# Kernel tuning notes

Measured on AMD Instinct MI355X. Metric: run time of the kernel, lower is better.

## Reference

```python
import jax, jax.numpy as jnp
import numpy as np
from jax import lax

LATENT_DIM = 512
TOKEN_DIM = 256
KERNEL = 5
STRIDE = 5


def setup_inputs() -> dict:
    key = jax.random.key(0)
    ks = jax.random.split(key, 8)
    B, L, S = 8, 1024, 10240
    s = lambda fan_in: 1.0 / np.sqrt(fan_in)
    return {
        "latents": jax.random.normal(ks[0], (B, L, LATENT_DIM), dtype=jnp.float32),
        "tokens": jax.random.normal(ks[1], (B, S, TOKEN_DIM), dtype=jnp.float32),
        # nn.Linear weights, stored as (out, in) like torch
        "W_lat": jax.random.uniform(ks[2], (LATENT_DIM, LATENT_DIM), jnp.float32, -s(LATENT_DIM), s(LATENT_DIM)),
        "W_tok": jax.random.uniform(ks[3], (LATENT_DIM, LATENT_DIM), jnp.float32, -s(LATENT_DIM), s(LATENT_DIM)),
        "W_vlat": jax.random.uniform(ks[4], (LATENT_DIM, LATENT_DIM), jnp.float32, -s(LATENT_DIM), s(LATENT_DIM)),
        "W_vtok": jax.random.uniform(ks[5], (LATENT_DIM, LATENT_DIM), jnp.float32, -s(LATENT_DIM), s(LATENT_DIM)),
        # Conv1d weight (out_ch, in_ch, k) and bias
        "conv_w": jax.random.uniform(ks[6], (LATENT_DIM, TOKEN_DIM, KERNEL), jnp.float32, -s(TOKEN_DIM * KERNEL), s(TOKEN_DIM * KERNEL)),
        "conv_b": jax.random.uniform(ks[7], (LATENT_DIM,), jnp.float32, -s(TOKEN_DIM * KERNEL), s(TOKEN_DIM * KERNEL)),
    }


def reference(latents, tokens, W_lat, W_tok, W_vlat, W_vtok, conv_w, conv_b):
    # Conv1d: (B,S,token_dim) -> (B,S//5,latent_dim)
    tok = lax.conv_general_dilated(
        tokens.transpose(0, 2, 1), conv_w, window_strides=(STRIDE,),
        padding="VALID", dimension_numbers=("NCH", "OIH", "NCH"))
    tok = (tok + conv_b[None, :, None]).transpose(0, 2, 1)  # (B, S', D)

    R_lat = jnp.einsum("bld,ed->ble", latents, W_lat)
    R_tok = jnp.einsum("bsd,ed->bse", tok, W_tok)
    V_lat = jnp.einsum("bld,ed->ble", latents, W_vlat)
    V_tok = jnp.einsum("bsd,ed->bse", tok, W_vtok)

    # shared score matrix, used for both row-wise and column-wise softmax
    A = jnp.einsum("ble,bse->bls", R_lat, R_tok) / jnp.sqrt(jnp.float32(LATENT_DIM))
    delta_lat = jnp.einsum("bls,bse->ble", jax.nn.softmax(A, axis=-1), V_tok)
    delta_tok = jnp.einsum("bls,ble->bse", jax.nn.softmax(A, axis=1), V_lat)

    updated_latents = latents + delta_lat
    updated_tokens = tok + delta_tok
    output = jnp.concatenate([updated_latents, updated_tokens], axis=1)
    return (updated_latents, updated_tokens, output)
```

## Files before the change

### kernel.cpp

```cpp
#include <hip/hip_runtime.h>
#include <math.h>

#define SCALEF 0.044194173824159216f

typedef __attribute__((ext_vector_type(8))) short bf16x8;
typedef __attribute__((ext_vector_type(4))) float f32x4;

static __device__ __forceinline__ unsigned short f2bf(float f) {
    union { float f; unsigned int i; } v; v.f = f;
    return (unsigned short)((v.i + 0x7fffu + ((v.i >> 16) & 1u)) >> 16);
}
static __device__ __forceinline__ float bf2f(unsigned short h) {
    union { unsigned int i; float f; } v; v.i = ((unsigned int)h) << 16;
    return v.f;
}
static __device__ __forceinline__ void gload16(const void* g, void* l) {
    __builtin_amdgcn_global_load_lds(
        (const __attribute__((address_space(1))) unsigned int*)g,
        (__attribute__((address_space(3))) unsigned int*)l, 16, 0, 0);
}
static __device__ __forceinline__ int swz(int l, int n) {
    return (l & 7) * (n >> 3) + (l >> 3);
}

__global__ __launch_bounds__(256) void cvt_tl(const float4* __restrict__ tok,
                                              const float4* __restrict__ lat,
                                              ushort4* __restrict__ tokd,
                                              ushort4* __restrict__ latd) {
    long t = blockIdx.x * 256L + threadIdx.x;
    #pragma unroll
    for (int k = 0; k < 5; ++k) {
        long i = t + k * 1048576L;
        float4 f = tok[i];
        ushort4 u; u.x = f2bf(f.x); u.y = f2bf(f.y); u.z = f2bf(f.z); u.w = f2bf(f.w);
        tokd[i] = u;
    }
    {
        float4 f = lat[t];
        ushort4 u; u.x = f2bf(f.x); u.y = f2bf(f.y); u.z = f2bf(f.z); u.w = f2bf(f.w);
        latd[t] = u;
    }
}

__global__ __launch_bounds__(256) void prep_rest(
    const float4* __restrict__ wl, const float4* __restrict__ wt,
    const float4* __restrict__ wvl, const float4* __restrict__ wvt,
    const float* __restrict__ cw,
    ushort4* __restrict__ wlb, ushort4* __restrict__ wtb,
    ushort4* __restrict__ wvlb, ushort4* __restrict__ wvtb,
    unsigned int* __restrict__ wpb)
{
    const long NW = 65536, NCV = 327680;
    for (long i = blockIdx.x * 256L + threadIdx.x; i < 4 * NW + NCV;
         i += gridDim.x * 256L) {
        long r = i;
        const float4* s = nullptr; ushort4* d = nullptr;
        if (r < NW) { s = wl; d = wlb; }
        else if ((r -= NW) < NW) { s = wt; d = wtb; }
        else if ((r -= NW) < NW) { s = wvl; d = wvlb; }
        else if ((r -= NW) < NW) { s = wvt; d = wvtb; }
        else {
            r -= NW;
            long e = r / 640, rr = r % 640, k = rr >> 7, c2 = rr & 127;
            unsigned int lo = f2bf(cw[e * 1280 + (2 * c2) * 5 + k]);
            unsigned int hi = f2bf(cw[e * 1280 + (2 * c2 + 1) * 5 + k]);
            wpb[r] = lo | (hi << 16);
            continue;
        }
        float4 f = s[r];
        ushort4 u; u.x = f2bf(f.x); u.y = f2bf(f.y); u.z = f2bf(f.z); u.w = f2bf(f.w);
        d[r] = u;
    }
}

template<int RL>
static __device__ __forceinline__ void sm_body(unsigned short* __restrict__ rowp,
                                               float* __restrict__ redm,
                                               float* __restrict__ reds) {
    constexpr int U = RL / 512;
    unsigned int* p = (unsigned int*)rowp;
    const int t = threadIdx.x, lane = t & 63, wid = t >> 6;
    unsigned int u[U];
    float v[2 * U];
    #pragma unroll
    for (int i = 0; i < U; ++i) u[i] = p[t + (i << 8)];
    #pragma unroll
    for (int i = 0; i < U; ++i) {
        v[2 * i]     = bf2f((unsigned short)(u[i] & 0xffffu));
        v[2 * i + 1] = bf2f((unsigned short)(u[i] >> 16));
    }
    float m = -INFINITY;
    #pragma unroll
    for (int i = 0; i < 2 * U; ++i) m = fmaxf(m, v[i]);
    #pragma unroll
    for (int k = 1; k < 64; k <<= 1) m = fmaxf(m, __shfl_xor(m, k));
    if (lane == 0) redm[wid] = m;
    __syncthreads();
    m = fmaxf(fmaxf(redm[0], redm[1]), fmaxf(redm[2], redm[3]));
    float s = 0.f, e[2 * U];
    #pragma unroll
    for (int i = 0; i < 2 * U; ++i) { e[i] = __expf(v[i] - m); s += e[i]; }
    #pragma unroll
    for (int k = 1; k < 64; k <<= 1) s += __shfl_xor(s, k);
    if (lane == 0) reds[wid] = s;
    __syncthreads();
    s = reds[0] + reds[1] + reds[2] + reds[3];
    float inv = 1.f / s;
    #pragma unroll
    for (int i = 0; i < U; ++i) {
        unsigned int lo = f2bf(e[2 * i] * inv);
        unsigned int hi = f2bf(e[2 * i + 1] * inv);
        p[t + (i << 8)] = lo | (hi << 16);
    }
}

__global__ __launch_bounds__(256) void softmax_both(unsigned short* __restrict__ S,
                                                    unsigned short* __restrict__ ST) {
    __shared__ float redm[4], reds[4];
    long b = blockIdx.x;
    if (b < 8192) sm_body<2048>(S + b * 2048L, redm, reds);
    else          sm_body<1024>(ST + (b - 8192) * 1024L, redm, reds);
}

template<int AMODE, int EPI>
static __device__ __forceinline__ void mm_body(
    char* __restrict__ smc, int bx, int by, int z,
    const unsigned short* __restrict__ A, const unsigned short* __restrict__ B,
    long bsA, long bsB, int lda, int ldb, int K,
    unsigned short* __restrict__ Cb, long bsCb,
    float* __restrict__ C0, long bsC0, float* __restrict__ C1, long bsC1,
    const void* __restrict__ basep, long bsBase, int ldc, float scale)
{
    const int t = threadIdx.x, lane = t & 63, wid = t >> 6;
    const int m0 = by << 7, n0 = bx << 7;
    const unsigned short* Ab = A + (long)z * bsA;
    const unsigned short* Bb = B + (long)z * bsB;

    const int rA0 = wid * 16 + (lane >> 2);
    const int rA1 = rA0 + 64;
    const int cs0 = (lane & 3) ^ ((rA0 >> 1) & 3);
    const int cs1 = (lane & 3) ^ ((rA1 >> 1) & 3);

    long aoff0, aoff1;
    if (AMODE == 0) {
        aoff0 = (long)(m0 + rA0) * lda + cs0 * 8;
        aoff1 = (long)(m0 + rA1) * lda + cs1 * 8;
    } else {
        int ma = m0 + rA0, mb = m0 + rA1;
        aoff0 = (long)(ma >> 11) * 2621440 + (long)(ma & 2047) * 1280 + cs0 * 8;
        aoff1 = (long)(mb >> 11) * 2621440 + (long)(mb & 2047) * 1280 + cs1 * 8;
    }
    const long boff0 = (long)(n0 + rA0) * ldb + cs0 * 8;
    const long boff1 = (long)(n0 + rA1) * ldb + cs1 * 8;

    const int dA0 = (wid << 10), dA1 = ((wid + 4) << 10);
    const int dB0 = 8192 + (wid << 10), dB1 = 8192 + ((wid + 4) << 10);

    const int wr = wid >> 1, wc = wid & 1;
    const int l15 = lane & 15, cslot = lane >> 4;
    int offA[4], offB[4];
    #pragma unroll
    for (int i = 0; i < 4; ++i) {
        int r = wr * 64 + i * 16 + l15;
        offA[i] = r * 64 + ((cslot ^ ((r >> 1) & 3)) << 4);
        int rb = wc * 64 + i * 16 + l15;
        offB[i] = 8192 + rb * 64 + ((cslot ^ ((rb >> 1) & 3)) << 4);
    }

    f32x4 acc[4][4];
    #pragma unroll
    for (int i = 0; i < 4; ++i)
        #pragma unroll
        for (int j = 0; j < 4; ++j)
            acc[i][j] = (f32x4)(0.f);

#define STAGE(p, ktv) do {                                   \
        int kb_ = (ktv);                                     \
        int bo_ = (p) * 16384;                               \
        gload16(Ab + aoff0 + kb_, smc + bo_ + dA0);          \
        gload16(Ab + aoff1 + kb_, smc + bo_ + dA1);          \
        gload16(Bb + boff0 + kb_, smc + bo_ + dB0);          \
        gload16(Bb + boff1 + kb_, smc + bo_ + dB1);          \
    } while (0)

    const int nt = K >> 5;
    STAGE(0, 0);
    STAGE(1, 32);
    int cur = 0;
    for (int it = 0; it < nt; ++it) {
        if (it + 2 < nt) {
            int nx2 = (cur >= 1) ? cur - 1 : 2;
            STAGE(nx2, (it + 2) << 5);
            asm volatile("s_waitcnt vmcnt(8)" ::: "memory");
        } else if (it + 1 < nt) {
            asm volatile("s_waitcnt vmcnt(4)" ::: "memory");
        } else {
            asm volatile("s_waitcnt vmcnt(0)" ::: "memory");
        }
        __builtin_amdgcn_s_barrier();
        const char* base = smc + cur * 16384;
        bf16x8 af[4], bfr[4];
        #pragma unroll
        for (int i = 0; i < 4; ++i) af[i]  = *(const bf16x8*)(base + offA[i]);
        #pragma unroll
        for (int i = 0; i < 4; ++i) bfr[i] = *(const bf16x8*)(base + offB[i]);
        #pragma unroll
        for (int i = 0; i < 4; ++i)
            #pragma unroll
            for (int j = 0; j < 4; ++j)
                acc[i][j] = __builtin_amdgcn_mfma_f32_16x16x32_bf16(af[i], bfr[j], acc[i][j], 0, 0, 0);
        asm volatile("s_waitcnt lgkmcnt(0)" ::: "memory");
        __builtin_amdgcn_s_barrier();
        cur = (cur + 1 == 3) ? 0 : cur + 1;
    }
#undef STAGE

    const int colb = n0 + wc * 64 + l15;
    const int rowb = m0 + wr * 64 + cslot * 4;
    if (EPI == 4) {
        unsigned short* STp = (unsigned short*)C0;
        #pragma unroll
        for (int i = 0; i < 4; ++i) {
            #pragma unroll
            for (int j = 0; j < 4; ++j) {
                int n = colb + j * 16;
                int mb = rowb + i * 16;
                float v0 = acc[i][j][0] * scale, v1 = acc[i][j][1] * scale;
                float v2 = acc[i][j][2] * scale, v3 = acc[i][j][3] * scale;
                unsigned short b0 = f2bf(v0), b1 = f2bf(v1), b2 = f2bf(v2), b3 = f2bf(v3);
                unsigned short* sp = Cb + (long)z * bsCb + (long)mb * ldc + n;
                sp[0] = b0; sp[ldc] = b1; sp[2 * ldc] = b2; sp[3 * ldc] = b3;
                ushort4 st4; st4.x = b0; st4.y = b1; st4.z = b2; st4.w = b3;
                *(ushort4*)(STp + (long)z * bsC0 + (long)n * bsC1 + mb) = st4;
            }
        }
        return;
    }
    #pragma unroll
    for (int i = 0; i < 4; ++i) {
        #pragma unroll
        for (int j = 0; j < 4; ++j) {
            int n = colb + j * 16;
            #pragma unroll
            for (int q = 0; q < 4; ++q) {
                int m = rowb + i * 16 + q;
                float v = acc[i][j][q];
                if (EPI == 0) {
                    Cb[(long)z * bsCb + (long)m * ldc + n] = f2bf(v * scale);
                } else if (EPI == 1) {
                    v += ((const float*)basep)[n];
                    Cb[(long)m * ldc + n] = f2bf(v);
                } else if (EPI == 2) {
                    float bv = ((const float*)basep)[(long)z * bsBase + (long)m * ldc + n];
                    float o = bv + v;
                    C0[(long)z * bsC0 + (long)m * ldc + n] = o;
                    C1[(long)z * bsC1 + (long)m * ldc + n] = o;
                } else {
                    float bv = bf2f(((const unsigned short*)basep)[(long)z * bsBase + (long)m * ldc + n]);
                    float o = bv + v;
                    C0[(long)z * bsC0 + (long)m * ldc + n] = o;
                    C1[(long)z * bsC1 + (long)m * ldc + n] = o;
                }
            }
        }
    }
}

__global__ __launch_bounds__(256) void gemm_g1(
    const unsigned short* __restrict__ tknb, const unsigned short* __restrict__ wpb,
    const float* __restrict__ conv_b, unsigned short* __restrict__ tokb,
    const unsigned short* __restrict__ latb, const unsigned short* __restrict__ wlb,
    unsigned short* __restrict__ rlat,
    const unsigned short* __restrict__ wvlb, unsigned short* __restrict__ vlT)
{
    __shared__ unsigned short sm[24576];
    char* smc = (char*)sm;
    const int bid = blockIdx.x;
    if (bid < 512) {
        int l = swz(bid, 512);
        mm_body<1, 1>(smc, l & 3, l >> 2, 0, tknb, wpb, 0, 0, 1280, 1280, 1280,
                      tokb, 0, nullptr, 0, nullptr, 0, conv_b, 0, 512, 1.f);
    } else if (bid < 768) {
        int l = swz(bid - 512, 256);
        mm_body<0, 0>(smc, l & 3, l >> 2, 0, latb, wlb, 0, 0, 512, 512, 512,
                      rlat, 0, nullptr, 0, nullptr, 0, nullptr, 0, 512, 1.f);
    } else {
        int l = swz(bid - 768, 256);
        mm_body<0, 0>(smc, l & 7, (l >> 3) & 3, l >> 5, wvlb, latb, 0, 524288,
                      512, 512, 512, vlT, 524288, nullptr, 0, nullptr, 0,
                      nullptr, 0, 1024, 1.f);
    }
}

__global__ __launch_bounds__(256) void gemm_g2(
    const unsigned short* __restrict__ tokb, const unsigned short* __restrict__ wtb,
    unsigned short* __restrict__ rtok,
    const unsigned short* __restrict__ wvtb, unsigned short* __restrict__ vtT)
{
    __shared__ unsigned short sm[24576];
    char* smc = (char*)sm;
    const int bid = blockIdx.x;
    if (bid < 512) {
        int l = swz(bid, 512);
        mm_body<0, 0>(smc, l & 3, l >> 2, 0, tokb, wtb, 0, 0, 512, 512, 512,
                      rtok, 0, nullptr, 0, nullptr, 0, nullptr, 0, 512, 1.f);
    } else {
        int l = swz(bid - 512, 512);
        mm_body<0, 0>(smc, l & 15, (l >> 4) & 3, l >> 6, wvtb, tokb, 0, 1048576,
                      512, 512, 512, vtT, 1048576, nullptr, 0, nullptr, 0,
                      nullptr, 0, 2048, 1.f);
    }
}

__global__ __launch_bounds__(256) void gemm_sc(
    const unsigned short* __restrict__ rlat, const unsigned short* __restrict__ rtok,
    unsigned short* __restrict__ S, unsigned short* __restrict__ ST)
{
    __shared__ unsigned short sm[24576];
    int l = swz((int)blockIdx.x, 1024);
    mm_body<0, 4>((char*)sm, l & 15, (l >> 4) & 7, l >> 7,
                  rlat, rtok, 524288, 1048576, 512, 512, 512,
                  S, 2097152, (float*)ST, 2097152, nullptr, 1024,
                  nullptr, 0, 2048, SCALEF);
}

__global__ __launch_bounds__(256) void gemm_g3(
    const unsigned short* __restrict__ S, const unsigned short* __restrict__ ST,
    const unsigned short* __restrict__ vlT, const unsigned short* __restrict__ vtT,
    const float* __restrict__ latents, const unsigned short* __restrict__ tokb,
    float* __restrict__ out)
{
    __shared__ unsigned short sm[24576];
    char* smc = (char*)sm;
    const int bid = blockIdx.x;
    if (bid < 256) {
        int l = swz(bid, 256);
        mm_body<0, 2>(smc, l & 3, (l >> 2) & 7, l >> 5, S, vtT, 2097152, 1048576,
                      2048, 2048, 2048, nullptr, 0,
                      out, 524288, out + 12582912, 1572864,
                      latents, 524288, 512, 1.f);
    } else {
        int l = swz(bid - 256, 512);
        mm_body<0, 3>(smc, l & 3, (l >> 2) & 15, l >> 6, ST, vlT, 2097152, 524288,
                      1024, 1024, 1024, nullptr, 0,
                      out + 4194304, 1048576, out + 12582912 + 524288, 1572864,
                      tokb, 1048576, 512, 1.f);
    }
}

extern "C" void kernel_launch(void* const* d_in, const int* in_sizes, int n_in,
                              void* d_out, int out_size, void* d_ws, size_t ws_size,
                              hipStream_t stream)
{
    const float* latents = (const float*)d_in[0];
    const float* tokens  = (const float*)d_in[1];
    const float* W_lat   = (const float*)d_in[2];
    const float* W_tok   = (const float*)d_in[3];
    const float* W_vlat  = (const float*)d_in[4];
    const float* W_vtok  = (const float*)d_in[5];
    const float* conv_w  = (const float*)d_in[6];
    const float* conv_b  = (const float*)d_in[7];
    float* out = (float*)d_out;
    char* ws = (char*)d_ws;

    unsigned short* S    = (unsigned short*)(ws);
    unsigned short* ST   = (unsigned short*)(ws + 33554432);
    unsigned short* tokb = (unsigned short*)(ws + 67108864);
    unsigned short* latb = (unsigned short*)(ws + 83886080);
    unsigned short* rlat = (unsigned short*)(ws + 92274688);
    unsigned short* rtok = (unsigned short*)(ws + 100663296);
    unsigned short* vlT  = (unsigned short*)(ws + 117440512);
    unsigned short* vtT  = (unsigned short*)(ws + 125829120);
    unsigned short* wpb  = (unsigned short*)(ws + 142606336);
    unsigned short* wlb  = (unsigned short*)(ws + 143917056);
    unsigned short* wtb  = (unsigned short*)(ws + 144441344);
    unsigned short* wvlb = (unsigned short*)(ws + 144965632);
    unsigned short* wvtb = (unsigned short*)(ws + 145489920);
    unsigned short* tknb = (unsigned short*)(out + 12582912);

    cvt_tl<<<4096, 256, 0, stream>>>((const float4*)tokens, (const float4*)latents,
                                     (ushort4*)tknb, (ushort4*)latb);
    prep_rest<<<512, 256, 0, stream>>>(
        (const float4*)W_lat, (const float4*)W_tok,
        (const float4*)W_vlat, (const float4*)W_vtok, conv_w,
        (ushort4*)wlb, (ushort4*)wtb, (ushort4*)wvlb, (ushort4*)wvtb,
        (unsigned int*)wpb);

    gemm_g1<<<1024, 256, 0, stream>>>(tknb, wpb, conv_b, tokb,
                                      latb, wlb, rlat, wvlb, vlT);

    gemm_g2<<<1024, 256, 0, stream>>>(tokb, wtb, rtok, wvtb, vtT);

    gemm_sc<<<1024, 256, 0, stream>>>(rlat, rtok, S, ST);

    softmax_both<<<24576, 256, 0, stream>>>(S, ST);

    gemm_g3<<<768, 256, 0, stream>>>(S, ST, vlT, vtT, latents, tokb, out);
}
```

Measured before the change: 226.6 us.

## Fold W_lat and W_tok into one matrix so scores use raw tokens

Rewrites the score computation algebraically: instead of projecting latents with W_lat and tokens with W_tok separately, it precomputes M = W_lat^T W_tok (from transposed bf16 weights), forms P = latents·M, and computes scores as P·tok. This removes the R_tok projection GEMM over the large token sequence and replaces it with a small 512x512 weight product plus a latent-sized GEMM, cutting total FLOPs and grid sizes. It adds an extra bf16 rounding step on M and P, which may change numerical error slightly, and the transposing weight conversion uses strided scalar loads.

```diff
diff --git a/kernel.cpp b/kernel.cpp
--- a/kernel.cpp
+++ b/kernel.cpp
@@ -43,10 +43,10 @@
 }
 
 __global__ __launch_bounds__(256) void prep_rest(
-    const float4* __restrict__ wl, const float4* __restrict__ wt,
+    const float* __restrict__ wl, const float* __restrict__ wt,
     const float4* __restrict__ wvl, const float4* __restrict__ wvt,
     const float* __restrict__ cw,
-    ushort4* __restrict__ wlb, ushort4* __restrict__ wtb,
+    ushort4* __restrict__ wlT, ushort4* __restrict__ wtT,
     ushort4* __restrict__ wvlb, ushort4* __restrict__ wvtb,
     unsigned int* __restrict__ wpb)
 {
@@ -54,10 +54,22 @@
     for (long i = blockIdx.x * 256L + threadIdx.x; i < 4 * NW + NCV;
          i += gridDim.x * 256L) {
         long r = i;
-        const float4* s = nullptr; ushort4* d = nullptr;
-        if (r < NW) { s = wl; d = wlb; }
-        else if ((r -= NW) < NW) { s = wt; d = wtb; }
-        else if ((r -= NW) < NW) { s = wvl; d = wvlb; }
+        if (r < 2 * NW) {
+            const float* src = (r < NW) ? wl : wt;
+            ushort4* dst = (r < NW) ? wlT : wtT;
+            long u = (r < NW) ? r : r - NW;
+            int a = (int)(u >> 7), e4 = (int)(u & 127);
+            ushort4 o;
+            o.x = f2bf(src[(e4 * 4 + 0) * 512 + a]);
+            o.y = f2bf(src[(e4 * 4 + 1) * 512 + a]);
+            o.z = f2bf(src[(e4 * 4 + 2) * 512 + a]);
+            o.w = f2bf(src[(e4 * 4 + 3) * 512 + a]);
+            dst[a * 128 + e4] = o;
+            continue;
+        }
+        r -= 2 * NW;
+        const float4* s; ushort4* d;
+        if (r < NW) { s = wvl; d = wvlb; }
         else if ((r -= NW) < NW) { s = wvt; d = wvtb; }
         else {
             r -= NW;
@@ -269,9 +281,10 @@
 __global__ __launch_bounds__(256) void gemm_g1(
     const unsigned short* __restrict__ tknb, const unsigned short* __restrict__ wpb,
     const float* __restrict__ conv_b, unsigned short* __restrict__ tokb,
-    const unsigned short* __restrict__ latb, const unsigned short* __restrict__ wlb,
-    unsigned short* __restrict__ rlat,
-    const unsigned short* __restrict__ wvlb, unsigned short* __restrict__ vlT)
+    const unsigned short* __restrict__ latb,
+    const unsigned short* __restrict__ wvlb, unsigned short* __restrict__ vlT,
+    const unsigned short* __restrict__ wtT, const unsigned short* __restrict__ wlT,
+    unsigned short* __restrict__ Mt)
 {
     __shared__ unsigned short sm[24576];
     char* smc = (char*)sm;
@@ -281,45 +294,46 @@
         mm_body<1, 1>(smc, l & 3, l >> 2, 0, tknb, wpb, 0, 0, 1280, 1280, 1280,
                       tokb, 0, nullptr, 0, nullptr, 0, conv_b, 0, 512, 1.f);
     } else if (bid < 768) {
-        int l = swz(bid - 512, 256);
-        mm_body<0, 0>(smc, l & 3, l >> 2, 0, latb, wlb, 0, 0, 512, 512, 512,
-                      rlat, 0, nullptr, 0, nullptr, 0, nullptr, 0, 512, 1.f);
-    } else {
-        int l = swz(bid - 768, 256);
+        int l = swz(bid - 768 + 256, 256);
         mm_body<0, 0>(smc, l & 7, (l >> 3) & 3, l >> 5, wvlb, latb, 0, 524288,
                       512, 512, 512, vlT, 524288, nullptr, 0, nullptr, 0,
                       nullptr, 0, 1024, 1.f);
+    } else {
+        int l = bid - 768;
+        mm_body<0, 0>(smc, l & 3, l >> 2, 0, wtT, wlT, 0, 0, 512, 512, 512,
+                      Mt, 0, nullptr, 0, nullptr, 0, nullptr, 0, 512, 1.f);
     }
 }
 
 __global__ __launch_bounds__(256) void gemm_g2(
-    const unsigned short* __restrict__ tokb, const unsigned short* __restrict__ wtb,
-    unsigned short* __restrict__ rtok,
-    const unsigned short* __restrict__ wvtb, unsigned short* __restrict__ vtT)
+    const unsigned short* __restrict__ tokb,
+    const unsigned short* __restrict__ wvtb, unsigned short* __restrict__ vtT,
+    const unsigned short* __restrict__ latb, const unsigned short* __restrict__ Mt,
+    unsigned short* __restrict__ P)
 {
     __shared__ unsigned short sm[24576];
     char* smc = (char*)sm;
     const int bid = blockIdx.x;
     if (bid < 512) {
         int l = swz(bid, 512);
-        mm_body<0, 0>(smc, l & 3, l >> 2, 0, tokb, wtb, 0, 0, 512, 512, 512,
-                      rtok, 0, nullptr, 0, nullptr, 0, nullptr, 0, 512, 1.f);
-    } else {
-        int l = swz(bid - 512, 512);
         mm_body<0, 0>(smc, l & 15, (l >> 4) & 3, l >> 6, wvtb, tokb, 0, 1048576,
                       512, 512, 512, vtT, 1048576, nullptr, 0, nullptr, 0,
                       nullptr, 0, 2048, 1.f);
+    } else {
+        int l = swz(bid - 512, 256);
+        mm_body<0, 0>(smc, l & 3, l >> 2, 0, latb, Mt, 0, 0, 512, 512, 512,
+                      P, 0, nullptr, 0, nullptr, 0, nullptr, 0, 512, 1.f);
     }
 }
 
 __global__ __launch_bounds__(256) void gemm_sc(
-    const unsigned short* __restrict__ rlat, const unsigned short* __restrict__ rtok,
+    const unsigned short* __restrict__ P, const unsigned short* __restrict__ tokb,
     unsigned short* __restrict__ S, unsigned short* __restrict__ ST)
 {
     __shared__ unsigned short sm[24576];
     int l = swz((int)blockIdx.x, 1024);
     mm_body<0, 4>((char*)sm, l & 15, (l >> 4) & 7, l >> 7,
-                  rlat, rtok, 524288, 1048576, 512, 512, 512,
+                  P, tokb, 524288, 1048576, 512, 512, 512,
                   S, 2097152, (float*)ST, 2097152, nullptr, 1024,
                   nullptr, 0, 2048, SCALEF);
 }
@@ -367,13 +381,13 @@
     unsigned short* ST   = (unsigned short*)(ws + 33554432);
     unsigned short* tokb = (unsigned short*)(ws + 67108864);
     unsigned short* latb = (unsigned short*)(ws + 83886080);
-    unsigned short* rlat = (unsigned short*)(ws + 92274688);
-    unsigned short* rtok = (unsigned short*)(ws + 100663296);
+    unsigned short* P    = (unsigned short*)(ws + 92274688);
+    unsigned short* Mt   = (unsigned short*)(ws + 100663296);
     unsigned short* vlT  = (unsigned short*)(ws + 117440512);
     unsigned short* vtT  = (unsigned short*)(ws + 125829120);
     unsigned short* wpb  = (unsigned short*)(ws + 142606336);
-    unsigned short* wlb  = (unsigned short*)(ws + 143917056);
-    unsigned short* wtb  = (unsigned short*)(ws + 144441344);
+    unsigned short* wlT  = (unsigned short*)(ws + 143917056);
+    unsigned short* wtT  = (unsigned short*)(ws + 144441344);
     unsigned short* wvlb = (unsigned short*)(ws + 144965632);
     unsigned short* wvtb = (unsigned short*)(ws + 145489920);
     unsigned short* tknb = (unsigned short*)(out + 12582912);
@@ -381,17 +395,16 @@
     cvt_tl<<<4096, 256, 0, stream>>>((const float4*)tokens, (const float4*)latents,
                                      (ushort4*)tknb, (ushort4*)latb);
     prep_rest<<<512, 256, 0, stream>>>(
-        (const float4*)W_lat, (const float4*)W_tok,
-        (const float4*)W_vlat, (const float4*)W_vtok, conv_w,
-        (ushort4*)wlb, (ushort4*)wtb, (ushort4*)wvlb, (ushort4*)wvtb,
+        W_lat, W_tok, (const float4*)W_vlat, (const float4*)W_vtok, conv_w,
+        (ushort4*)wlT, (ushort4*)wtT, (ushort4*)wvlb, (ushort4*)wvtb,
         (unsigned int*)wpb);
 
-    gemm_g1<<<1024, 256, 0, stream>>>(tknb, wpb, conv_b, tokb,
-                                      latb, wlb, rlat, wvlb, vlT);
-
-    gemm_g2<<<1024, 256, 0, stream>>>(tokb, wtb, rtok, wvtb, vtT);
-
-    gemm_sc<<<1024, 256, 0, stream>>>(rlat, rtok, S, ST);
+    gemm_g1<<<784, 256, 0, stream>>>(tknb, wpb, conv_b, tokb,
+                                     latb, wvlb, vlT, wtT, wlT, Mt);
+
+    gemm_g2<<<768, 256, 0, stream>>>(tokb, wvtb, vtT, latb, Mt, P);
+
+    gemm_sc<<<1024, 256, 0, stream>>>(P, tokb, S, ST);
 
     softmax_both<<<24576, 256, 0, stream>>>(S, ST);
 
```

Result: no change. 227.6 us (+0.4%).
